# Kernel optimization log

Measured on AMD Instinct MI355X. Metric: run time of the kernel, lower is better.

The kernel has to match this reference:

```python
import jax, jax.numpy as jnp
import numpy as np

N = 50000      # total nodes
E = 800000     # total edges
B = 512        # number of graphs (batch size)
D_IN, H, D_OUT = 5, 96, 192
EPS = 1e-5


def setup_inputs() -> dict:
    key = jax.random.key(0)
    ks = jax.random.split(key, 20)
    s = lambda d: 1.0 / np.sqrt(d)
    inp = {
        "x": jax.random.normal(ks[0], (N, D_IN), jnp.float32),
        "edge_index": jax.random.randint(ks[1], (2, E), 0, N, jnp.int64),
        "batch": jnp.sort(jax.random.randint(ks[2], (N,), 0, B, jnp.int64)),
        "W_in": jax.random.normal(ks[3], (D_IN, H), jnp.float32) * s(D_IN),
        "b_in": jnp.zeros((H,), jnp.float32),
        "W1": jax.random.normal(ks[4], (H, H), jnp.float32) * s(H),
        "b1": jnp.zeros((H,), jnp.float32),
        "g1": jnp.ones((H,), jnp.float32),
        "be1": jnp.zeros((H,), jnp.float32),
        "W2": jax.random.normal(ks[5], (H, H), jnp.float32) * s(H),
        "b2": jnp.zeros((H,), jnp.float32),
        "g2": jnp.ones((H,), jnp.float32),
        "be2": jnp.zeros((H,), jnp.float32),
        "W_out": jax.random.normal(ks[6], (H, D_OUT), jnp.float32) * s(H),
        "b_out": jnp.zeros((D_OUT,), jnp.float32),
        "ln_g": jnp.ones((D_OUT,), jnp.float32),
        "ln_b": jnp.zeros((D_OUT,), jnp.float32),
    }
    return inp


def gcn_conv(h, W, b, src, dst):
    # PyG GCNConv: h' = D^{-1/2} (A + I) D^{-1/2} (h W) + b, deg from self-looped graph
    h = h @ W                                           # [N, H]
    deg = jnp.ones((N,), h.dtype).at[dst].add(jnp.ones((E,), h.dtype))
    dinv = jax.lax.rsqrt(deg)                           # [N]
    coef = dinv[src] * dinv[dst]                        # [E]
    agg = jnp.zeros_like(h).at[dst].add(h[src] * coef[:, None])
    agg = agg + h * (dinv * dinv)[:, None]              # self-loop term
    return agg + b


def batch_norm(x, g, b):
    m = x.mean(0)
    v = x.var(0)
    return g * (x - m) * jax.lax.rsqrt(v + EPS) + b


def reference(x, edge_index, batch, W_in, b_in, W1, b1, g1, be1, W2, b2, g2, be2,
              W_out, b_out, ln_g, ln_b):
    src, dst = edge_index[0], edge_index[1]
    h = jax.nn.relu(x @ W_in + b_in)
    for (W, bb, g, be) in ((W1, b1, g1, be1), (W2, b2, g2, be2)):
        r = h
        h = gcn_conv(h, W, bb, src, dst)
        h = jax.nn.relu(batch_norm(h, g, be))           # dropout = identity (eval)
        h = h + r
    counts = jnp.zeros((B,), h.dtype).at[batch].add(1.0)
    pooled = jax.ops.segment_sum(h, batch, num_segments=B)
    pooled = pooled / jnp.maximum(counts, 1.0)[:, None]  # global_mean_pool [B, H]
    out = pooled @ W_out + b_out                         # [B, D_OUT]
    mu = out.mean(-1, keepdims=True)
    var = out.var(-1, keepdims=True)
    return ln_g * (out - mu) * jax.lax.rsqrt(var + EPS) + ln_b
```

## Files before the change

kernel.cpp:

```cpp
#include <hip/hip_runtime.h>
#include <hip/hip_bf16.h>
#include <stdint.h>

#define NN 50000
#define EE 800000
#define BB 512
#define HH 96
#define DIN 5
#define DOUT 192
#define EPSV 1e-5f
#define NBANK 32
#define HWS 48
#define NB_GATHER 3125
#define NBLK_SCAN ((NN + 1023) / 1024)
#define NBUK 512
#define BUKN 98
#define FILLB 128
#define FCHUNK (EE / FILLB)

__device__ inline float blo(uint32_t w) { return __uint_as_float(w << 16); }
__device__ inline float bhi(uint32_t w) { return __uint_as_float(w & 0xffff0000u); }
__device__ inline uint32_t packbf(float a, float b) {
    uint32_t ua = __float_as_uint(a); ua += 0x7fffu + ((ua >> 16) & 1u);
    uint32_t ub = __float_as_uint(b); ub += 0x7fffu + ((ub >> 16) & 1u);
    return (ua >> 16) | (ub & 0xffff0000u);
}

__global__ __launch_bounds__(256) void k_bhist(const int* __restrict__ dst,
                                               int* __restrict__ bkcnt) {
    __shared__ int hist[NBUK];
    int tid = threadIdx.x;
    for (int j = tid; j < NBUK; j += 256) hist[j] = 0;
    __syncthreads();
    int e0 = blockIdx.x * FCHUNK;
    for (int e = e0 + tid; e < e0 + FCHUNK; e += 256) atomicAdd(&hist[dst[e] / BUKN], 1);
    __syncthreads();
    for (int j = tid; j < NBUK; j += 256) if (hist[j]) atomicAdd(&bkcnt[j], hist[j]);
}

__global__ __launch_bounds__(256) void k_bscan(const int* __restrict__ bkcnt,
                                               int* __restrict__ bkbase,
                                               int* __restrict__ bkcur,
                                               float* __restrict__ stats,
                                               int* __restrict__ row_ptr) {
    __shared__ int sc[NBUK + 1];
    int t = threadIdx.x;
    for (int i = t; i < 2 * NBANK * 192; i += 256) stats[i] = 0.0f;
    for (int j = t; j < NBUK; j += 256) sc[j] = bkcnt[j];
    __syncthreads();
    if (t == 0) {
        int c = 0;
        for (int j = 0; j < NBUK; ++j) { int s = sc[j]; sc[j] = c; c += s; }
        sc[NBUK] = c;
        row_ptr[NN] = c;
    }
    __syncthreads();
    for (int j = t; j <= NBUK; j += 256) bkbase[j] = sc[j];
    for (int j = t; j < NBUK; j += 256) bkcur[j] = sc[j];
}

__global__ __launch_bounds__(256) void k_bscat(const int* __restrict__ src,
                                               const int* __restrict__ dst,
                                               int* __restrict__ bkcur,
                                               uint32_t* __restrict__ ebuf) {
    __shared__ int hist[NBUK], bbase[NBUK], cnt[NBUK];
    int tid = threadIdx.x;
    int e0 = blockIdx.x * FCHUNK, e1 = e0 + FCHUNK;
    for (int j = tid; j < NBUK; j += 256) { hist[j] = 0; cnt[j] = 0; }
    __syncthreads();
    for (int e = e0 + tid; e < e1; e += 256) atomicAdd(&hist[dst[e] / BUKN], 1);
    __syncthreads();
    for (int j = tid; j < NBUK; j += 256) bbase[j] = hist[j] ? atomicAdd(&bkcur[j], hist[j]) : 0;
    __syncthreads();
    for (int e = e0 + tid; e < e1; e += 256) {
        int d = dst[e];
        int b = d / BUKN;
        int off = atomicAdd(&cnt[b], 1);
        ebuf[bbase[b] + off] = (uint32_t)src[e] | ((uint32_t)(d - b * BUKN) << 16);
    }
}

__global__ __launch_bounds__(256) void k_csr(const uint32_t* __restrict__ ebuf,
                                             const int* __restrict__ bkbase,
                                             int* __restrict__ row_ptr,
                                             int* __restrict__ col,
                                             int* __restrict__ degi,
                                             float* __restrict__ dinv) {
    __shared__ int cnt[BUKN], base[BUKN], lcur[BUKN];
    int b = blockIdx.x, tid = threadIdx.x;
    int node0 = b * BUKN;
    if (node0 >= NN) return;
    int nn = min(BUKN, NN - node0);
    int ebase = bkbase[b], eend = bkbase[b + 1];
    for (int j = tid; j < nn; j += 256) { cnt[j] = 0; lcur[j] = 0; }
    __syncthreads();
    for (int i = ebase + tid; i < eend; i += 256) atomicAdd(&cnt[ebuf[i] >> 16], 1);
    __syncthreads();
    if (tid == 0) {
        int c = 0;
        for (int j = 0; j < nn; ++j) { base[j] = c; c += cnt[j]; }
    }
    __syncthreads();
    for (int j = tid; j < nn; j += 256) {
        row_ptr[node0 + j] = ebase + base[j];
        degi[node0 + j] = cnt[j];
        dinv[node0 + j] = rsqrtf((float)cnt[j] + 1.0f);
    }
    for (int i = ebase + tid; i < eend; i += 256) {
        uint32_t w = ebuf[i];
        int dr = (int)(w >> 16);
        int off = atomicAdd(&lcur[dr], 1);
        col[ebase + base[dr] + off] = (int)(w & 0xffffu);
    }
}

__global__ __launch_bounds__(1024) void k_dhist(const int* __restrict__ degi,
                                                int* __restrict__ histg) {
    __shared__ int dh[64];
    int tid = threadIdx.x;
    if (tid < 64) dh[tid] = 0;
    __syncthreads();
    int i = blockIdx.x * 1024 + tid;
    if (i < NN) atomicAdd(&dh[min(degi[i], 63)], 1);
    __syncthreads();
    if (tid < 64) histg[blockIdx.x * 64 + tid] = dh[tid];
}

__global__ __launch_bounds__(64) void k_dscan(int* __restrict__ histg) {
    __shared__ int tot[64], binbase[64];
    int t = threadIdx.x;
    int s = 0;
    for (int k = 0; k < NBLK_SCAN; ++k) s += histg[k * 64 + t];
    tot[t] = s;
    __syncthreads();
    if (t == 0) {
        int c = 0;
        for (int b2 = 0; b2 < 64; ++b2) { binbase[b2] = c; c += tot[b2]; }
    }
    __syncthreads();
    int c = binbase[t];
    for (int k = 0; k < NBLK_SCAN; ++k) {
        int tmp = histg[k * 64 + t];
        histg[k * 64 + t] = c;
        c += tmp;
    }
}

__global__ __launch_bounds__(1024) void k_dperm(const int* __restrict__ degi,
                                                const int* __restrict__ histg,
                                                int* __restrict__ perm) {
    __shared__ int lcur[64];
    int tid = threadIdx.x;
    if (tid < 64) lcur[tid] = histg[blockIdx.x * 64 + tid];
    __syncthreads();
    int i = blockIdx.x * 1024 + tid;
    if (i < NN) {
        int pos = atomicAdd(&lcur[min(degi[i], 63)], 1);
        perm[pos] = i;
    }
}

__device__ inline void pack24(uint32_t* __restrict__ dstrow, int q,
                              const float* v, float scale) {
    uint32_t wv[12];
#pragma unroll
    for (int p = 0; p < 12; ++p) wv[p] = packbf(v[2 * p] * scale, v[2 * p + 1] * scale);
    uint4* dstp = reinterpret_cast<uint4*>(dstrow + q * 12);
    dstp[0] = make_uint4(wv[0], wv[1], wv[2], wv[3]);
    dstp[1] = make_uint4(wv[4], wv[5], wv[6], wv[7]);
    dstp[2] = make_uint4(wv[8], wv[9], wv[10], wv[11]);
}

__global__ __launch_bounds__(256) void k_gemm_in(const float* __restrict__ x,
                                                 const float* __restrict__ Win,
                                                 const float* __restrict__ bin,
                                                 const float* __restrict__ W1,
                                                 const float* __restrict__ dinv,
                                                 uint32_t* __restrict__ h0b,
                                                 uint32_t* __restrict__ hwb) {
    __shared__ float sAT[96][68];
    __shared__ float sW[96 * 96];
    int tid = threadIdx.x;
    int row0 = blockIdx.x * 64;

    for (int i = tid; i < 96 * 96; i += 256) sW[i] = W1[i];

    {
        int r = tid >> 2, q = tid & 3;
        int j0q = q * 24;
        int gr = row0 + r;
        float xv[5];
#pragma unroll
        for (int k = 0; k < DIN; ++k) xv[k] = (gr < NN) ? x[gr * DIN + k] : 0.0f;
        float hv[24];
#pragma unroll
        for (int jj = 0; jj < 24; ++jj) {
            float acc = bin[j0q + jj];
#pragma unroll
            for (int k = 0; k < DIN; ++k) acc += xv[k] * Win[k * 96 + j0q + jj];
            hv[jj] = fmaxf(acc, 0.0f);
            sAT[j0q + jj][r] = hv[jj];
        }
        if (gr < NN) pack24(&h0b[(size_t)gr * HWS], q, hv, 1.0f);
    }
    __syncthreads();

    int tc = tid & 15, tr = tid >> 4;
    int r0 = tr * 4, j0 = tc * 6;
    float acc[4][6];
#pragma unroll
    for (int i = 0; i < 4; ++i)
#pragma unroll
        for (int j = 0; j < 6; ++j) acc[i][j] = 0.0f;

    for (int k = 0; k < 96; ++k) {
        float4 a = *reinterpret_cast<const float4*>(&sAT[k][r0]);
        const float* wr = &sW[k * 96 + j0];
        float b0 = wr[0], b1 = wr[1], b2 = wr[2], b3 = wr[3], b4 = wr[4], b5 = wr[5];
        float av[4] = {a.x, a.y, a.z, a.w};
#pragma unroll
        for (int i = 0; i < 4; ++i) {
            acc[i][0] += av[i] * b0; acc[i][1] += av[i] * b1; acc[i][2] += av[i] * b2;
            acc[i][3] += av[i] * b3; acc[i][4] += av[i] * b4; acc[i][5] += av[i] * b5;
        }
    }
#pragma unroll
    for (int i = 0; i < 4; ++i) {
        int gr = row0 + r0 + i;
        if (gr < NN) {
            float dv = dinv[gr];
            uint32_t* wp = &hwb[(size_t)gr * HWS + tc * 3];
            wp[0] = packbf(acc[i][0] * dv, acc[i][1] * dv);
            wp[1] = packbf(acc[i][2] * dv, acc[i][3] * dv);
            wp[2] = packbf(acc[i][4] * dv, acc[i][5] * dv);
        }
    }
}

__global__ __launch_bounds__(256) void k_gather(const uint32_t* __restrict__ hwb,
                                                const float* __restrict__ dinv,
                                                const int* __restrict__ row_ptr,
                                                const int* __restrict__ col,
                                                const int* __restrict__ perm,
                                                uint32_t* __restrict__ aggb,
                                                float* __restrict__ stats) {
    int tid = threadIdx.x;
    int t = tid & 15, slot = tid >> 4;
    int n = perm[blockIdx.x * 16 + slot];

    const uint32_t* rn = hwb + (size_t)n * HWS;
    uint2 w01 = *reinterpret_cast<const uint2*>(rn + 2 * t);
    uint32_t w2 = rn[32 + t];
    float a0 = blo(w01.x), a1 = bhi(w01.x);
    float a2 = blo(w01.y), a3 = bhi(w01.y);
    float a4 = blo(w2),    a5 = bhi(w2);

    int beg = row_ptr[n], end = row_ptr[n + 1];
    int p = beg;
    for (; p + 3 < end; p += 4) {
        int s0 = col[p], s1 = col[p + 1], s2 = col[p + 2], s3 = col[p + 3];
        const uint32_t* r0 = hwb + (size_t)s0 * HWS;
        const uint32_t* r1 = hwb + (size_t)s1 * HWS;
        const uint32_t* r2 = hwb + (size_t)s2 * HWS;
        const uint32_t* r3 = hwb + (size_t)s3 * HWS;
        uint2 u0 = *reinterpret_cast<const uint2*>(r0 + 2 * t); uint32_t v0 = r0[32 + t];
        uint2 u1 = *reinterpret_cast<const uint2*>(r1 + 2 * t); uint32_t v1 = r1[32 + t];
        uint2 u2 = *reinterpret_cast<const uint2*>(r2 + 2 * t); uint32_t v2 = r2[32 + t];
        uint2 u3 = *reinterpret_cast<const uint2*>(r3 + 2 * t); uint32_t v3 = r3[32 + t];
        a0 += blo(u0.x); a1 += bhi(u0.x); a2 += blo(u0.y); a3 += bhi(u0.y);
        a4 += blo(v0);   a5 += bhi(v0);
        a0 += blo(u1.x); a1 += bhi(u1.x); a2 += blo(u1.y); a3 += bhi(u1.y);
        a4 += blo(v1);   a5 += bhi(v1);
        a0 += blo(u2.x); a1 += bhi(u2.x); a2 += blo(u2.y); a3 += bhi(u2.y);
        a4 += blo(v2);   a5 += bhi(v2);
        a0 += blo(u3.x); a1 += bhi(u3.x); a2 += blo(u3.y); a3 += bhi(u3.y);
        a4 += blo(v3);   a5 += bhi(v3);
    }
    for (; p < end; ++p) {
        const uint32_t* rs = hwb + (size_t)col[p] * HWS;
        uint2 u = *reinterpret_cast<const uint2*>(rs + 2 * t);
        uint32_t v = rs[32 + t];
        a0 += blo(u.x); a1 += bhi(u.x);
        a2 += blo(u.y); a3 += bhi(u.y);
        a4 += blo(v);   a5 += bhi(v);
    }
    float dn = dinv[n];
    a0 *= dn; a1 *= dn; a2 *= dn; a3 *= dn; a4 *= dn; a5 *= dn;

    uint32_t* an = aggb + (size_t)n * HWS;
    *reinterpret_cast<uint2*>(an + 2 * t) = make_uint2(packbf(a0, a1), packbf(a2, a3));
    an[32 + t] = packbf(a4, a5);

    __shared__ float red[2][96];
    if (tid < 96) { red[0][tid] = 0.0f; red[1][tid] = 0.0f; }
    __syncthreads();
    int colsv[6] = {4 * t, 4 * t + 1, 4 * t + 2, 4 * t + 3, 64 + 2 * t, 64 + 2 * t + 1};
    float cs[6] = {a0, a1, a2, a3, a4, a5};
#pragma unroll
    for (int k = 0; k < 6; ++k) {
        atomicAdd(&red[0][colsv[k]], cs[k]);
        atomicAdd(&red[1][colsv[k]], cs[k] * cs[k]);
    }
    __syncthreads();
    float* bank = stats + (blockIdx.x & (NBANK - 1)) * 192;
    if (tid < 96) {
        atomicAdd(&bank[tid], red[0][tid]);
        atomicAdd(&bank[96 + tid], red[1][tid]);
    }
}

__global__ __launch_bounds__(256) void k_gemm_bn(const uint32_t* __restrict__ aggb,
                                                 const uint32_t* __restrict__ hprevb,
                                                 const float* __restrict__ stats,
                                                 const float* __restrict__ g,
                                                 const float* __restrict__ be,
                                                 const float* __restrict__ W,
                                                 const float* __restrict__ dinv,
                                                 uint32_t* __restrict__ hnewb,
                                                 uint32_t* __restrict__ hwb) {
    __shared__ float sAT[96][68];
    __shared__ float sW[96 * 96];
    __shared__ float ssc[96], ssh[96];
    int tid = threadIdx.x;
    int row0 = blockIdx.x * 64;

    for (int i = tid; i < 96 * 96; i += 256) sW[i] = W[i];
    if (tid < 96) {
        float s = 0.0f, s2 = 0.0f;
#pragma unroll
        for (int k = 0; k < NBANK; ++k) { s += stats[k * 192 + tid]; s2 += stats[k * 192 + 96 + tid]; }
        float m = s * (1.0f / NN);
        float var = s2 * (1.0f / NN) - m * m;
        float sc = g[tid] * rsqrtf(var + EPSV);
        ssc[tid] = sc;
        ssh[tid] = be[tid] - m * sc;
    }
    __syncthreads();

    for (int i = tid; i < 64 * 24; i += 256) {
        int r = i / 24, qq = i % 24;
        int gr = row0 + r, c = qq * 4, w0 = qq * 2;
        float v0 = 0.0f, v1 = 0.0f, v2 = 0.0f, v3 = 0.0f;
        if (gr < NN) {
            uint2 aw = *reinterpret_cast<const uint2*>(&aggb[(size_t)gr * HWS + w0]);
            uint2 pw = *reinterpret_cast<const uint2*>(&hprevb[(size_t)gr * HWS + w0]);
            v0 = fmaxf(blo(aw.x) * ssc[c]     + ssh[c],     0.0f) + blo(pw.x);
            v1 = fmaxf(bhi(aw.x) * ssc[c + 1] + ssh[c + 1], 0.0f) + bhi(pw.x);
            v2 = fmaxf(blo(aw.y) * ssc[c + 2] + ssh[c + 2], 0.0f) + blo(pw.y);
            v3 = fmaxf(bhi(aw.y) * ssc[c + 3] + ssh[c + 3], 0.0f) + bhi(pw.y);
            *reinterpret_cast<uint2*>(&hnewb[(size_t)gr * HWS + w0]) =
                make_uint2(packbf(v0, v1), packbf(v2, v3));
        }
        sAT[c][r] = v0; sAT[c + 1][r] = v1; sAT[c + 2][r] = v2; sAT[c + 3][r] = v3;
    }
    __syncthreads();

    int tc = tid & 15, tr = tid >> 4;
    int r0 = tr * 4, j0 = tc * 6;
    float acc[4][6];
#pragma unroll
    for (int i = 0; i < 4; ++i)
#pragma unroll
        for (int j = 0; j < 6; ++j) acc[i][j] = 0.0f;

    for (int k = 0; k < 96; ++k) {
        float4 a = *reinterpret_cast<const float4*>(&sAT[k][r0]);
        const float* wr = &sW[k * 96 + j0];
        float b0 = wr[0], b1 = wr[1], b2 = wr[2], b3 = wr[3], b4 = wr[4], b5 = wr[5];
        float av[4] = {a.x, a.y, a.z, a.w};
#pragma unroll
        for (int i = 0; i < 4; ++i) {
            acc[i][0] += av[i] * b0; acc[i][1] += av[i] * b1; acc[i][2] += av[i] * b2;
            acc[i][3] += av[i] * b3; acc[i][4] += av[i] * b4; acc[i][5] += av[i] * b5;
        }
    }
#pragma unroll
    for (int i = 0; i < 4; ++i) {
        int gr = row0 + r0 + i;
        if (gr < NN) {
            float dv = dinv[gr];
            uint32_t* wp = &hwb[(size_t)gr * HWS + tc * 3];
            wp[0] = packbf(acc[i][0] * dv, acc[i][1] * dv);
            wp[1] = packbf(acc[i][2] * dv, acc[i][3] * dv);
            wp[2] = packbf(acc[i][4] * dv, acc[i][5] * dv);
        }
    }
}

__device__ inline int lower_bound_i(const int* __restrict__ a, int n, int v) {
    int lo = 0, hi = n;
    while (lo < hi) { int mid = (lo + hi) >> 1; if (a[mid] < v) lo = mid + 1; else hi = mid; }
    return lo;
}

__global__ __launch_bounds__(384) void k_out(const uint32_t* __restrict__ aggb,
                                             const uint32_t* __restrict__ hprevb,
                                             const float* __restrict__ stats,
                                             const float* __restrict__ g,
                                             const float* __restrict__ be,
                                             const int* __restrict__ batch,
                                             const float* __restrict__ Wout,
                                             const float* __restrict__ bout,
                                             const float* __restrict__ lg,
                                             const float* __restrict__ lb,
                                             float* __restrict__ out) {
    __shared__ float ssc[96], ssh[96];
    __shared__ float sp8[8][96];
    __shared__ float sp[96];
    __shared__ float svals[192];
    __shared__ float smv[2];
    int b = blockIdx.x, t = threadIdx.x;
    if (t < 96) {
        float s = 0.0f, s2 = 0.0f;
#pragma unroll
        for (int k = 0; k < NBANK; ++k) { s += stats[k * 192 + t]; s2 += stats[k * 192 + 96 + t]; }
        float m = s * (1.0f / NN);
        float var = s2 * (1.0f / NN) - m * m;
        float sc = g[t] * rsqrtf(var + EPSV);
        ssc[t] = sc;
        ssh[t] = be[t] - m * sc;
    }
    int lo = lower_bound_i(batch, NN, b);
    int hi = lower_bound_i(batch, NN, b + 1);
    __syncthreads();

    int w = t % 48, qr = t / 48;
    int c0 = 2 * w, c1 = 2 * w + 1;
    float sc0 = ssc[c0], sh0 = ssh[c0], sc1 = ssc[c1], sh1 = ssh[c1];
    float accp0 = 0.0f, accp1 = 0.0f;
    for (int r = lo + qr; r < hi; r += 8) {
        uint32_t a = aggb[(size_t)r * HWS + w];
        uint32_t h = hprevb[(size_t)r * HWS + w];
        accp0 += fmaxf(blo(a) * sc0 + sh0, 0.0f) + blo(h);
        accp1 += fmaxf(bhi(a) * sc1 + sh1, 0.0f) + bhi(h);
    }
    sp8[qr][c0] = accp0;
    sp8[qr][c1] = accp1;
    __syncthreads();
    if (t < 96) {
        float inv = (hi > lo) ? 1.0f / (float)(hi - lo) : 0.0f;
        float s = 0.0f;
#pragma unroll
        for (int k = 0; k < 8; ++k) s += sp8[k][t];
        sp[t] = s * inv;
    }
    __syncthreads();

    float acc = 0.0f;
    if (t < 192) {
        acc = bout[t];
        for (int k = 0; k < 96; ++k) acc += sp[k] * Wout[k * 192 + t];
        svals[t] = acc;
    }
    __syncthreads();
    if (t < 64) {
        float a0 = svals[t], a1 = svals[t + 64], a2 = svals[t + 128];
        float s = a0 + a1 + a2;
        float s2 = a0 * a0 + a1 * a1 + a2 * a2;
        for (int o = 32; o > 0; o >>= 1) {
            s += __shfl_down(s, o, 64);
            s2 += __shfl_down(s2, o, 64);
        }
        if (t == 0) { smv[0] = s * (1.0f / 192.0f); smv[1] = s2 * (1.0f / 192.0f); }
    }
    __syncthreads();
    if (t < 192) {
        float m = smv[0];
        float var = smv[1] - m * m;
        float rr = rsqrtf(var + EPSV);
        out[b * 192 + t] = lg[t] * (acc - m) * rr + lb[t];
    }
}

extern "C" void kernel_launch(void* const* d_in, const int* in_sizes, int n_in,
                              void* d_out, int out_size, void* d_ws, size_t ws_size,
                              hipStream_t stream) {
    const float* x    = (const float*)d_in[0];
    const int*   ei   = (const int*)  d_in[1];
    const int*   batch= (const int*)  d_in[2];
    const float* Win  = (const float*)d_in[3];
    const float* bin  = (const float*)d_in[4];
    const float* W1   = (const float*)d_in[5];
    const float* g1   = (const float*)d_in[7];
    const float* be1  = (const float*)d_in[8];
    const float* W2   = (const float*)d_in[9];
    const float* g2   = (const float*)d_in[11];
    const float* be2  = (const float*)d_in[12];
    const float* Wout = (const float*)d_in[13];
    const float* bout = (const float*)d_in[14];
    const float* lg   = (const float*)d_in[15];
    const float* lb   = (const float*)d_in[16];
    const int* src = ei;
    const int* dst = ei + EE;

    uint32_t* wsp    = (uint32_t*)d_ws;
    uint32_t* h0b    = wsp;
    uint32_t* h1b    = h0b + (size_t)NN * HWS;
    uint32_t* aggb   = h1b + (size_t)NN * HWS;
    uint32_t* hwb    = aggb + (size_t)NN * HWS;
    float*    dinv   = (float*)(hwb + (size_t)NN * HWS);
    float*    stats  = dinv + NN;
    int*      degi   = (int*)(stats + 2 * NBANK * 192);
    int*      histg  = degi + NN;
    int*      row_ptr= histg + NBLK_SCAN * 64;
    int*      perm   = row_ptr + NN + 1;
    int*      bkcnt  = perm + NN;
    int*      bkbase = bkcnt + NBUK;
    int*      bkcur  = bkbase + NBUK + 1;
    int*      col    = bkcur + NBUK;
    uint32_t* ebuf   = aggb;

    const int TB = 256;
    float* stats1 = stats;
    float* stats2 = stats + NBANK * 192;

    hipMemsetAsync(bkcnt, 0, NBUK * sizeof(int), stream);
    k_bhist<<<FILLB, TB, 0, stream>>>(dst, bkcnt);
    k_bscan<<<1, TB, 0, stream>>>(bkcnt, bkbase, bkcur, stats, row_ptr);
    k_bscat<<<FILLB, TB, 0, stream>>>(src, dst, bkcur, ebuf);
    k_csr<<<NBUK, TB, 0, stream>>>(ebuf, bkbase, row_ptr, col, degi, dinv);
    k_dhist<<<NBLK_SCAN, 1024, 0, stream>>>(degi, histg);
    k_dscan<<<1, 64, 0, stream>>>(histg);
    k_dperm<<<NBLK_SCAN, 1024, 0, stream>>>(degi, histg, perm);

    k_gemm_in<<<(NN + 63) / 64, TB, 0, stream>>>(x, Win, bin, W1, dinv, h0b, hwb);
    k_gather<<<NB_GATHER, TB, 0, stream>>>(hwb, dinv, row_ptr, col, perm, aggb, stats1);

    k_gemm_bn<<<(NN + 63) / 64, TB, 0, stream>>>(aggb, h0b, stats1, g1, be1, W2, dinv, h1b, hwb);
    k_gather<<<NB_GATHER, TB, 0, stream>>>(hwb, dinv, row_ptr, col, perm, aggb, stats2);

    k_out<<<BB, 384, 0, stream>>>(aggb, h1b, stats2, g2, be2, batch, Wout, bout, lg, lb,
                                  (float*)d_out);
}
```

Baseline: 258.0 us.

## Fuse CSR preprocessing stages and recompute input embedding instead of storing it

The edge bucketing now keeps per-block histograms and scans them, so the scatter kernel no longer recounts edges or uses global atomics, and the memset is removed. The degree histogram is built inside the CSR kernel, which drops the separate degree-histogram kernel. The scan and permutation kernels now work per bucket. The bf16 h0 buffer is no longer written; the second GEMM recomputes relu(x@W_in+b_in) from x, trading extra arithmetic for less memory traffic. This removes a launch and a 9.6MB write plus read, but the scan kernel now loops serially over 128 blocks, and the degree scan over 512 entries is longer.

Measured after the change: 263.6 us. +2.1%, slower.

```diff
diff --git a/kernel.cpp b/kernel.cpp
--- a/kernel.cpp
+++ b/kernel.cpp
@@ -12,7 +12,6 @@
 #define NBANK 32
 #define HWS 48
 #define NB_GATHER 3125
-#define NBLK_SCAN ((NN + 1023) / 1024)
 #define NBUK 512
 #define BUKN 98
 #define FILLB 128
@@ -27,7 +26,7 @@
 }
 
 __global__ __launch_bounds__(256) void k_bhist(const int* __restrict__ dst,
-                                               int* __restrict__ bkcnt) {
+                                               int* __restrict__ histgb) {
     __shared__ int hist[NBUK];
     int tid = threadIdx.x;
     for (int j = tid; j < NBUK; j += 256) hist[j] = 0;
@@ -35,43 +34,50 @@
     int e0 = blockIdx.x * FCHUNK;
     for (int e = e0 + tid; e < e0 + FCHUNK; e += 256) atomicAdd(&hist[dst[e] / BUKN], 1);
     __syncthreads();
-    for (int j = tid; j < NBUK; j += 256) if (hist[j]) atomicAdd(&bkcnt[j], hist[j]);
-}
-
-__global__ __launch_bounds__(256) void k_bscan(const int* __restrict__ bkcnt,
+    for (int j = tid; j < NBUK; j += 256) histgb[blockIdx.x * NBUK + j] = hist[j];
+}
+
+__global__ __launch_bounds__(512) void k_bscan(int* __restrict__ histgb,
                                                int* __restrict__ bkbase,
-                                               int* __restrict__ bkcur,
                                                float* __restrict__ stats,
                                                int* __restrict__ row_ptr) {
-    __shared__ int sc[NBUK + 1];
+    __shared__ int sc[NBUK];
     int t = threadIdx.x;
-    for (int i = t; i < 2 * NBANK * 192; i += 256) stats[i] = 0.0f;
-    for (int j = t; j < NBUK; j += 256) sc[j] = bkcnt[j];
+    for (int i = t; i < 2 * NBANK * 192; i += 512) stats[i] = 0.0f;
+    {
+        int c = 0;
+        for (int b = 0; b < FILLB; ++b) {
+            int idx = b * NBUK + t;
+            int tmp = histgb[idx];
+            histgb[idx] = c;
+            c += tmp;
+        }
+        sc[t] = c;
+    }
     __syncthreads();
     if (t == 0) {
         int c = 0;
         for (int j = 0; j < NBUK; ++j) { int s = sc[j]; sc[j] = c; c += s; }
-        sc[NBUK] = c;
         row_ptr[NN] = c;
-    }
-    __syncthreads();
-    for (int j = t; j <= NBUK; j += 256) bkbase[j] = sc[j];
-    for (int j = t; j < NBUK; j += 256) bkcur[j] = sc[j];
+        bkbase[NBUK] = c;
+    }
+    __syncthreads();
+    bkbase[t] = sc[t];
 }
 
 __global__ __launch_bounds__(256) void k_bscat(const int* __restrict__ src,
                                                const int* __restrict__ dst,
-                                               int* __restrict__ bkcur,
+                                               const int* __restrict__ histgb,
+                                               const int* __restrict__ bkbase,
                                                uint32_t* __restrict__ ebuf) {
-    __shared__ int hist[NBUK], bbase[NBUK], cnt[NBUK];
+    __shared__ int bbase[NBUK], cnt[NBUK];
     int tid = threadIdx.x;
+    for (int j = tid; j < NBUK; j += 256) {
+        bbase[j] = bkbase[j] + histgb[blockIdx.x * NBUK + j];
+        cnt[j] = 0;
+    }
+    __syncthreads();
     int e0 = blockIdx.x * FCHUNK, e1 = e0 + FCHUNK;
-    for (int j = tid; j < NBUK; j += 256) { hist[j] = 0; cnt[j] = 0; }
-    __syncthreads();
-    for (int e = e0 + tid; e < e1; e += 256) atomicAdd(&hist[dst[e] / BUKN], 1);
-    __syncthreads();
-    for (int j = tid; j < NBUK; j += 256) bbase[j] = hist[j] ? atomicAdd(&bkcur[j], hist[j]) : 0;
-    __syncthreads();
     for (int e = e0 + tid; e < e1; e += 256) {
         int d = dst[e];
         int b = d / BUKN;
@@ -85,13 +91,19 @@
                                              int* __restrict__ row_ptr,
                                              int* __restrict__ col,
                                              int* __restrict__ degi,
-                                             float* __restrict__ dinv) {
+                                             float* __restrict__ dinv,
+                                             int* __restrict__ dhistb) {
     __shared__ int cnt[BUKN], base[BUKN], lcur[BUKN];
+    __shared__ int dh[64];
     int b = blockIdx.x, tid = threadIdx.x;
     int node0 = b * BUKN;
-    if (node0 >= NN) return;
+    if (node0 >= NN) {
+        if (tid < 64) dhistb[b * 64 + tid] = 0;
+        return;
+    }
     int nn = min(BUKN, NN - node0);
     int ebase = bkbase[b], eend = bkbase[b + 1];
+    if (tid < 64) dh[tid] = 0;
     for (int j = tid; j < nn; j += 256) { cnt[j] = 0; lcur[j] = 0; }
     __syncthreads();
     for (int i = ebase + tid; i < eend; i += 256) atomicAdd(&cnt[ebuf[i] >> 16], 1);
@@ -105,6 +117,7 @@
         row_ptr[node0 + j] = ebase + base[j];
         degi[node0 + j] = cnt[j];
         dinv[node0 + j] = rsqrtf((float)cnt[j] + 1.0f);
+        atomicAdd(&dh[min(cnt[j], 63)], 1);
     }
     for (int i = ebase + tid; i < eend; i += 256) {
         uint32_t w = ebuf[i];
@@ -112,63 +125,45 @@
         int off = atomicAdd(&lcur[dr], 1);
         col[ebase + base[dr] + off] = (int)(w & 0xffffu);
     }
-}
-
-__global__ __launch_bounds__(1024) void k_dhist(const int* __restrict__ degi,
-                                                int* __restrict__ histg) {
-    __shared__ int dh[64];
-    int tid = threadIdx.x;
-    if (tid < 64) dh[tid] = 0;
-    __syncthreads();
-    int i = blockIdx.x * 1024 + tid;
-    if (i < NN) atomicAdd(&dh[min(degi[i], 63)], 1);
-    __syncthreads();
-    if (tid < 64) histg[blockIdx.x * 64 + tid] = dh[tid];
-}
-
-__global__ __launch_bounds__(64) void k_dscan(int* __restrict__ histg) {
+    __syncthreads();
+    if (tid < 64) dhistb[b * 64 + tid] = dh[tid];
+}
+
+__global__ __launch_bounds__(64) void k_dscan(int* __restrict__ dhistb) {
     __shared__ int tot[64], binbase[64];
     int t = threadIdx.x;
     int s = 0;
-    for (int k = 0; k < NBLK_SCAN; ++k) s += histg[k * 64 + t];
+    for (int b = 0; b < NBUK; ++b) s += dhistb[b * 64 + t];
     tot[t] = s;
     __syncthreads();
     if (t == 0) {
         int c = 0;
-        for (int b2 = 0; b2 < 64; ++b2) { binbase[b2] = c; c += tot[b2]; }
+        for (int k = 0; k < 64; ++k) { binbase[k] = c; c += tot[k]; }
     }
     __syncthreads();
     int c = binbase[t];
-    for (int k = 0; k < NBLK_SCAN; ++k) {
-        int tmp = histg[k * 64 + t];
-        histg[k * 64 + t] = c;
+    for (int b = 0; b < NBUK; ++b) {
+        int tmp = dhistb[b * 64 + t];
+        dhistb[b * 64 + t] = c;
         c += tmp;
     }
 }
 
-__global__ __launch_bounds__(1024) void k_dperm(const int* __restrict__ degi,
-                                                const int* __restrict__ histg,
-                                                int* __restrict__ perm) {
+__global__ __launch_bounds__(128) void k_dperm(const int* __restrict__ degi,
+                                               const int* __restrict__ dhistb,
+                                               int* __restrict__ perm) {
     __shared__ int lcur[64];
-    int tid = threadIdx.x;
-    if (tid < 64) lcur[tid] = histg[blockIdx.x * 64 + tid];
-    __syncthreads();
-    int i = blockIdx.x * 1024 + tid;
-    if (i < NN) {
+    int b = blockIdx.x, t = threadIdx.x;
+    int node0 = b * BUKN;
+    if (node0 >= NN) return;
+    int nn = min(BUKN, NN - node0);
+    if (t < 64) lcur[t] = dhistb[b * 64 + t];
+    __syncthreads();
+    if (t < nn) {
+        int i = node0 + t;
         int pos = atomicAdd(&lcur[min(degi[i], 63)], 1);
         perm[pos] = i;
     }
-}
-
-__device__ inline void pack24(uint32_t* __restrict__ dstrow, int q,
-                              const float* v, float scale) {
-    uint32_t wv[12];
-#pragma unroll
-    for (int p = 0; p < 12; ++p) wv[p] = packbf(v[2 * p] * scale, v[2 * p + 1] * scale);
-    uint4* dstp = reinterpret_cast<uint4*>(dstrow + q * 12);
-    dstp[0] = make_uint4(wv[0], wv[1], wv[2], wv[3]);
-    dstp[1] = make_uint4(wv[4], wv[5], wv[6], wv[7]);
-    dstp[2] = make_uint4(wv[8], wv[9], wv[10], wv[11]);
 }
 
 __global__ __launch_bounds__(256) void k_gemm_in(const float* __restrict__ x,
@@ -176,7 +171,6 @@
                                                  const float* __restrict__ bin,
                                                  const float* __restrict__ W1,
                                                  const float* __restrict__ dinv,
-                                                 uint32_t* __restrict__ h0b,
                                                  uint32_t* __restrict__ hwb) {
     __shared__ float sAT[96][68];
     __shared__ float sW[96 * 96];
@@ -192,16 +186,13 @@
         float xv[5];
 #pragma unroll
         for (int k = 0; k < DIN; ++k) xv[k] = (gr < NN) ? x[gr * DIN + k] : 0.0f;
-        float hv[24];
 #pragma unroll
         for (int jj = 0; jj < 24; ++jj) {
             float acc = bin[j0q + jj];
 #pragma unroll
             for (int k = 0; k < DIN; ++k) acc += xv[k] * Win[k * 96 + j0q + jj];
-            hv[jj] = fmaxf(acc, 0.0f);
-            sAT[j0q + jj][r] = hv[jj];
-        }
-        if (gr < NN) pack24(&h0b[(size_t)gr * HWS], q, hv, 1.0f);
+            sAT[j0q + jj][r] = fmaxf(acc, 0.0f);
+        }
     }
     __syncthreads();
 
@@ -310,7 +301,9 @@
 }
 
 __global__ __launch_bounds__(256) void k_gemm_bn(const uint32_t* __restrict__ aggb,
-                                                 const uint32_t* __restrict__ hprevb,
+                                                 const float* __restrict__ x,
+                                                 const float* __restrict__ Win,
+                                                 const float* __restrict__ bin,
                                                  const float* __restrict__ stats,
                                                  const float* __restrict__ g,
                                                  const float* __restrict__ be,
@@ -320,12 +313,22 @@
                                                  uint32_t* __restrict__ hwb) {
     __shared__ float sAT[96][68];
     __shared__ float sW[96 * 96];
+    __shared__ float sx[64][6];
+    __shared__ float sWin[5 * 96];
+    __shared__ float sbin[96];
     __shared__ float ssc[96], ssh[96];
     int tid = threadIdx.x;
     int row0 = blockIdx.x * 64;
 
     for (int i = tid; i < 96 * 96; i += 256) sW[i] = W[i];
+    for (int i = tid; i < 5 * 96; i += 256) sWin[i] = Win[i];
+    for (int i = tid; i < 64 * 5; i += 256) {
+        int r = i / 5, k2 = i % 5;
+        int gr = row0 + r;
+        sx[r][k2] = (gr < NN) ? x[gr * DIN + k2] : 0.0f;
+    }
     if (tid < 96) {
+        sbin[tid] = bin[tid];
         float s = 0.0f, s2 = 0.0f;
 #pragma unroll
         for (int k = 0; k < NBANK; ++k) { s += stats[k * 192 + tid]; s2 += stats[k * 192 + 96 + tid]; }
@@ -343,11 +346,18 @@
         float v0 = 0.0f, v1 = 0.0f, v2 = 0.0f, v3 = 0.0f;
         if (gr < NN) {
             uint2 aw = *reinterpret_cast<const uint2*>(&aggb[(size_t)gr * HWS + w0]);
-            uint2 pw = *reinterpret_cast<const uint2*>(&hprevb[(size_t)gr * HWS + w0]);
-            v0 = fmaxf(blo(aw.x) * ssc[c]     + ssh[c],     0.0f) + blo(pw.x);
-            v1 = fmaxf(bhi(aw.x) * ssc[c + 1] + ssh[c + 1], 0.0f) + bhi(pw.x);
-            v2 = fmaxf(blo(aw.y) * ssc[c + 2] + ssh[c + 2], 0.0f) + blo(pw.y);
-            v3 = fmaxf(bhi(aw.y) * ssc[c + 3] + ssh[c + 3], 0.0f) + bhi(pw.y);
+            float hv[4];
+#pragma unroll
+            for (int u = 0; u < 4; ++u) {
+                float a = sbin[c + u];
+#pragma unroll
+                for (int k2 = 0; k2 < 5; ++k2) a += sx[r][k2] * sWin[k2 * 96 + c + u];
+                hv[u] = fmaxf(a, 0.0f);
+            }
+            v0 = fmaxf(blo(aw.x) * ssc[c]     + ssh[c],     0.0f) + hv[0];
+            v1 = fmaxf(bhi(aw.x) * ssc[c + 1] + ssh[c + 1], 0.0f) + hv[1];
+            v2 = fmaxf(blo(aw.y) * ssc[c + 2] + ssh[c + 2], 0.0f) + hv[2];
+            v3 = fmaxf(bhi(aw.y) * ssc[c + 3] + ssh[c + 3], 0.0f) + hv[3];
             *reinterpret_cast<uint2*>(&hnewb[(size_t)gr * HWS + w0]) =
                 make_uint2(packbf(v0, v1), packbf(v2, v3));
         }
@@ -494,39 +504,36 @@
     const int* dst = ei + EE;
 
     uint32_t* wsp    = (uint32_t*)d_ws;
-    uint32_t* h0b    = wsp;
-    uint32_t* h1b    = h0b + (size_t)NN * HWS;
+    uint32_t* h1b    = wsp;
     uint32_t* aggb   = h1b + (size_t)NN * HWS;
     uint32_t* hwb    = aggb + (size_t)NN * HWS;
     float*    dinv   = (float*)(hwb + (size_t)NN * HWS);
     float*    stats  = dinv + NN;
     int*      degi   = (int*)(stats + 2 * NBANK * 192);
-    int*      histg  = degi + NN;
-    int*      row_ptr= histg + NBLK_SCAN * 64;
+    int*      dhistb = degi + NN;
+    int*      row_ptr= dhistb + NBUK * 64;
     int*      perm   = row_ptr + NN + 1;
-    int*      bkcnt  = perm + NN;
-    int*      bkbase = bkcnt + NBUK;
-    int*      bkcur  = bkbase + NBUK + 1;
-    int*      col    = bkcur + NBUK;
+    int*      bkbase = perm + NN;
+    int*      histgb = bkbase + NBUK + 1;
+    int*      col    = histgb + FILLB * NBUK;
     uint32_t* ebuf   = aggb;
 
     const int TB = 256;
     float* stats1 = stats;
     float* stats2 = stats + NBANK * 192;
 
-    hipMemsetAsync(bkcnt, 0, NBUK * sizeof(int), stream);
-    k_bhist<<<FILLB, TB, 0, stream>>>(dst, bkcnt);
-    k_bscan<<<1, TB, 0, stream>>>(bkcnt, bkbase, bkcur, stats, row_ptr);
-    k_bscat<<<FILLB, TB, 0, stream>>>(src, dst, bkcur, ebuf);
-    k_csr<<<NBUK, TB, 0, stream>>>(ebuf, bkbase, row_ptr, col, degi, dinv);
-    k_dhist<<<NBLK_SCAN, 1024, 0, stream>>>(degi, histg);
-    k_dscan<<<1, 64, 0, stream>>>(histg);
-    k_dperm<<<NBLK_SCAN, 1024, 0, stream>>>(degi, histg, perm);
-
-    k_gemm_in<<<(NN + 63) / 64, TB, 0, stream>>>(x, Win, bin, W1, dinv, h0b, hwb);
+    k_bhist<<<FILLB, TB, 0, stream>>>(dst, histgb);
+    k_bscan<<<1, 512, 0, stream>>>(histgb, bkbase, stats, row_ptr);
+    k_bscat<<<FILLB, TB, 0, stream>>>(src, dst, histgb, bkbase, ebuf);
+    k_csr<<<NBUK, TB, 0, stream>>>(ebuf, bkbase, row_ptr, col, degi, dinv, dhistb);
+    k_dscan<<<1, 64, 0, stream>>>(dhistb);
+    k_dperm<<<NBUK, 128, 0, stream>>>(degi, dhistb, perm);
+
+    k_gemm_in<<<(NN + 63) / 64, TB, 0, stream>>>(x, Win, bin, W1, dinv, hwb);
     k_gather<<<NB_GATHER, TB, 0, stream>>>(hwb, dinv, row_ptr, col, perm, aggb, stats1);
 
-    k_gemm_bn<<<(NN + 63) / 64, TB, 0, stream>>>(aggb, h0b, stats1, g1, be1, W2, dinv, h1b, hwb);
+    k_gemm_bn<<<(NN + 63) / 64, TB, 0, stream>>>(aggb, x, Win, bin, stats1, g1, be1, W2,
+                                                 dinv, h1b, hwb);
     k_gather<<<NB_GATHER, TB, 0, stream>>>(hwb, dinv, row_ptr, col, perm, aggb, stats2);
 
     k_out<<<BB, 384, 0, stream>>>(aggb, h1b, stats2, g2, be2, batch, Wout, bout, lg, lb,
```
